# Kernel optimization log

Hardware: AMD Instinct MI355X
Metric: run time of the kernel (lower is better)

Reference implementation:

```python
import jax, jax.numpy as jnp
import numpy as np

P, S, C, F, B = 2, 2, 64, 64, 64


def setup_inputs() -> dict:
    key = jax.random.key(0)
    kx, kq, kw = jax.random.split(key, 3)
    X = jax.random.normal(kx, (B, P * S * C * F), dtype=jnp.float32)
    # sparse connection-strength tensor, densified; nonnegative small values
    dbfc = jax.random.uniform(kq, (P, S, C, F, C, F), dtype=jnp.float32) * 0.01
    wV = jax.random.normal(kw, (F, F), dtype=jnp.float32) * (1.0 / np.sqrt(F))
    return {"X": X, "databaseFeatureConnections": dbfc, "wV": wV}


def reference(X, databaseFeatureConnections, wV):
    p, s, c, f = (databaseFeatureConnections.shape[0], databaseFeatureConnections.shape[1],
                  databaseFeatureConnections.shape[2], databaseFeatureConnections.shape[3])
    b = X.shape[0]
    # wV: nn.Linear(f, f, bias=False) -> x @ W.T
    v = (X.reshape(b, p * s * c, f) @ wV.T).reshape(b, p, s, c, f)
    # kqHead.sum(dim=1).sum(dim=2): collapse both feature axes -> [p, s, c, c]
    scores = databaseFeatureConnections.sum(axis=(3, 5))
    weights = jax.nn.softmax(scores, axis=-1)  # [p, s, c, c]
    # per-head bmm: weights[p,s] @ v[:,p,s] -> [b, c, f] per head; heads concatenated
    # along feature dim in (p outer, s inner) order == reshape of [b, c, p, s, f]
    out = jnp.einsum('pscd,bpsdf->bcpsf', weights, v).reshape(b, c, p * s * f)
    # permute(1, 0, 2) -> [c, b, p*s*f]
    return out.transpose(1, 0, 2)
```

## Files before the change

### kernel.cpp

```cpp
#include <hip/hip_runtime.h>
#include <math.h>


__global__ __launch_bounds__(1024) void scores_softmax_kernel(
    const float* __restrict__ dbfc, float* __restrict__ weights)
{
    const int bid = blockIdx.x;
    const int t   = threadIdx.x;
    const float4* slab = reinterpret_cast<const float4*>(dbfc) + (size_t)bid * (262144 / 4);

    float acc = 0.f;
#pragma unroll 8
    for (int f = 0; f < 64; ++f) {
        float4 v = slab[f * 1024 + t];
        acc += (v.x + v.y) + (v.z + v.w);
    }
#pragma unroll
    for (int m = 1; m < 16; m <<= 1)
        acc += __shfl_xor(acc, m, 64);

    __shared__ float sm[64];
    if ((t & 15) == 0) sm[t >> 4] = acc;
    __syncthreads();

    if (t < 64) {
        float v = sm[t];
        float mx = v;
#pragma unroll
        for (int m = 32; m >= 1; m >>= 1) mx = fmaxf(mx, __shfl_xor(mx, m, 64));
        float e = expf(v - mx);
        float s = e;
#pragma unroll
        for (int m = 32; m >= 1; m >>= 1) s += __shfl_xor(s, m, 64);
        weights[bid * 64 + t] = e / s;
    }
}

__global__ __launch_bounds__(256) void attn_out_kernel(
    const float* __restrict__ X, const float* __restrict__ wV,
    const float* __restrict__ weights, float* __restrict__ out)
{
    const int blk = blockIdx.x;
    const int ps  = blk >> 6;
    const int b   = blk & 63;
    const int t   = threadIdx.x;
    const int tc  = t >> 4;
    const int tf  = t & 15;

    __shared__ float Xs [64][68];
    __shared__ float wVs[64][68];
    __shared__ float Ws [64][68];
    __shared__ float VsT[64][68];

    const float4* xsrc = reinterpret_cast<const float4*>(X + (size_t)b * 16384 + ps * 4096);
    const float4* wsrc = reinterpret_cast<const float4*>(wV);
    const float4* ssrc = reinterpret_cast<const float4*>(weights + ps * 4096);
#pragma unroll
    for (int idx = t; idx < 1024; idx += 256) {
        int r = idx >> 4, j = (idx & 15) * 4;
        *reinterpret_cast<float4*>(&Xs [r][j]) = xsrc[idx];
        *reinterpret_cast<float4*>(&wVs[r][j]) = wsrc[idx];
        *reinterpret_cast<float4*>(&Ws [r][j]) = ssrc[idx];
    }
    __syncthreads();

    float acc[4][4] = {};
    for (int f0 = 0; f0 < 64; f0 += 4) {
        float4 xa[4], wv[4];
#pragma unroll
        for (int ci = 0; ci < 4; ++ci)
            xa[ci] = *reinterpret_cast<const float4*>(&Xs[4 * tc + ci][f0]);
#pragma unroll
        for (int fi = 0; fi < 4; ++fi)
            wv[fi] = *reinterpret_cast<const float4*>(&wVs[tf + 16 * fi][f0]);
#pragma unroll
        for (int ci = 0; ci < 4; ++ci)
#pragma unroll
            for (int fi = 0; fi < 4; ++fi)
                acc[ci][fi] += xa[ci].x * wv[fi].x + xa[ci].y * wv[fi].y
                             + xa[ci].z * wv[fi].z + xa[ci].w * wv[fi].w;
    }
#pragma unroll
    for (int ci = 0; ci < 4; ++ci)
#pragma unroll
        for (int fi = 0; fi < 4; ++fi)
            VsT[tf + 16 * fi][4 * tc + ci] = acc[ci][fi];
    __syncthreads();

    float o[4][4] = {};
    for (int d = 0; d < 64; d += 4) {
        float4 wa[4], va[4];
#pragma unroll
        for (int ci = 0; ci < 4; ++ci)
            wa[ci] = *reinterpret_cast<const float4*>(&Ws[4 * tc + ci][d]);
#pragma unroll
        for (int fi = 0; fi < 4; ++fi)
            va[fi] = *reinterpret_cast<const float4*>(&VsT[tf + 16 * fi][d]);
#pragma unroll
        for (int ci = 0; ci < 4; ++ci)
#pragma unroll
            for (int fi = 0; fi < 4; ++fi)
                o[ci][fi] += wa[ci].x * va[fi].x + wa[ci].y * va[fi].y
                           + wa[ci].z * va[fi].z + wa[ci].w * va[fi].w;
    }

#pragma unroll
    for (int ci = 0; ci < 4; ++ci) {
        const int c = 4 * tc + ci;
        float* orow = out + ((size_t)c * 64 + b) * 256 + ps * 64;
#pragma unroll
        for (int fi = 0; fi < 4; ++fi)
            orow[tf + 16 * fi] = o[ci][fi];
    }
}

extern "C" void kernel_launch(void* const* d_in, const int* in_sizes, int n_in,
                              void* d_out, int out_size, void* d_ws, size_t ws_size,
                              hipStream_t stream)
{
    const float* X    = (const float*)d_in[0];
    const float* dbfc = (const float*)d_in[1];
    const float* wV   = (const float*)d_in[2];
    float* out        = (float*)d_out;
    float* weights    = (float*)d_ws;

    scores_softmax_kernel<<<256, 1024, 0, stream>>>(dbfc, weights);
    attn_out_kernel<<<256, 256, 0, stream>>>(X, wV, weights, out);
}
```

Measured before the change: 64.97 us.

## Split score reduction across more blocks with atomics and move softmax into attention kernel

The dbfc reduction is split from 256 blocks of 1024 threads into 2048 blocks of 256 threads. Each block reduces one chunk with four independent float4 accumulators and atomically adds its partial sums into a zeroed score buffer. The softmax moves into the attention kernel and runs on the shared-memory score tile. This aims to spread the 64 MB streaming read over more CUs and raise memory-level parallelism. The cost is an extra memset launch, float atomics with nondeterministic summation order, and softmax work repeated in every attention block.

Measured after the change: 59.91 us. 7.8% less time.

```diff
diff --git a/kernel.cpp b/kernel.cpp
--- a/kernel.cpp
+++ b/kernel.cpp
@@ -2,43 +2,52 @@
 #include <math.h>
 
 
-__global__ __launch_bounds__(1024) void scores_softmax_kernel(
-    const float* __restrict__ dbfc, float* __restrict__ weights)
+__global__ __launch_bounds__(256) void scores_partial_kernel(
+    const float* __restrict__ dbfc, float* __restrict__ scores)
 {
-    const int bid = blockIdx.x;
-    const int t   = threadIdx.x;
-    const float4* slab = reinterpret_cast<const float4*>(dbfc) + (size_t)bid * (262144 / 4);
+    const int bid   = blockIdx.x;
+    const int slab  = bid >> 3;
+    const int chunk = bid & 7;
+    const int t     = threadIdx.x;
 
-    float acc = 0.f;
-#pragma unroll 8
-    for (int f = 0; f < 64; ++f) {
-        float4 v = slab[f * 1024 + t];
-        acc += (v.x + v.y) + (v.z + v.w);
+    const float4* src = reinterpret_cast<const float4*>(dbfc)
+                      + (size_t)slab * 65536 + chunk * 8192 + t;
+
+    float4 a0 = make_float4(0.f, 0.f, 0.f, 0.f), a1 = a0, a2 = a0, a3 = a0;
+#pragma unroll 2
+    for (int i = 0; i < 32; i += 4) {
+        float4 v0 = src[(i + 0) * 256];
+        float4 v1 = src[(i + 1) * 256];
+        float4 v2 = src[(i + 2) * 256];
+        float4 v3 = src[(i + 3) * 256];
+        a0.x += v0.x; a0.y += v0.y; a0.z += v0.z; a0.w += v0.w;
+        a1.x += v1.x; a1.y += v1.y; a1.z += v1.z; a1.w += v1.w;
+        a2.x += v2.x; a2.y += v2.y; a2.z += v2.z; a2.w += v2.w;
+        a3.x += v3.x; a3.y += v3.y; a3.z += v3.z; a3.w += v3.w;
     }
+    float s0 = (a0.x + a0.y) + (a0.z + a0.w);
+    float s1 = (a1.x + a1.y) + (a1.z + a1.w);
+    float s2 = (a2.x + a2.y) + (a2.z + a2.w);
+    float s3 = (a3.x + a3.y) + (a3.z + a3.w);
 #pragma unroll
-    for (int m = 1; m < 16; m <<= 1)
-        acc += __shfl_xor(acc, m, 64);
-
-    __shared__ float sm[64];
-    if ((t & 15) == 0) sm[t >> 4] = acc;
-    __syncthreads();
-
-    if (t < 64) {
-        float v = sm[t];
-        float mx = v;
-#pragma unroll
-        for (int m = 32; m >= 1; m >>= 1) mx = fmaxf(mx, __shfl_xor(mx, m, 64));
-        float e = expf(v - mx);
-        float s = e;
-#pragma unroll
-        for (int m = 32; m >= 1; m >>= 1) s += __shfl_xor(s, m, 64);
-        weights[bid * 64 + t] = e / s;
+    for (int m = 1; m < 16; m <<= 1) {
+        s0 += __shfl_xor(s0, m, 64);
+        s1 += __shfl_xor(s1, m, 64);
+        s2 += __shfl_xor(s2, m, 64);
+        s3 += __shfl_xor(s3, m, 64);
+    }
+    if ((t & 15) == 0) {
+        float* dst = scores + slab * 64 + (t >> 4);
+        atomicAdd(dst +  0, s0);
+        atomicAdd(dst + 16, s1);
+        atomicAdd(dst + 32, s2);
+        atomicAdd(dst + 48, s3);
     }
 }
 
 __global__ __launch_bounds__(256) void attn_out_kernel(
     const float* __restrict__ X, const float* __restrict__ wV,
-    const float* __restrict__ weights, float* __restrict__ out)
+    const float* __restrict__ scores, float* __restrict__ out)
 {
     const int blk = blockIdx.x;
     const int ps  = blk >> 6;
@@ -54,7 +63,7 @@
 
     const float4* xsrc = reinterpret_cast<const float4*>(X + (size_t)b * 16384 + ps * 4096);
     const float4* wsrc = reinterpret_cast<const float4*>(wV);
-    const float4* ssrc = reinterpret_cast<const float4*>(weights + ps * 4096);
+    const float4* ssrc = reinterpret_cast<const float4*>(scores + ps * 4096);
 #pragma unroll
     for (int idx = t; idx < 1024; idx += 256) {
         int r = idx >> 4, j = (idx & 15) * 4;
@@ -80,6 +89,25 @@
                 acc[ci][fi] += xa[ci].x * wv[fi].x + xa[ci].y * wv[fi].y
                              + xa[ci].z * wv[fi].z + xa[ci].w * wv[fi].w;
     }
+
+    {
+        const int row = t >> 2, q = (t & 3) * 16;
+        float e[16];
+        float mx = -INFINITY;
+#pragma unroll
+        for (int i = 0; i < 16; ++i) mx = fmaxf(mx, Ws[row][q + i]);
+        mx = fmaxf(mx, __shfl_xor(mx, 1, 64));
+        mx = fmaxf(mx, __shfl_xor(mx, 2, 64));
+        float sum = 0.f;
+#pragma unroll
+        for (int i = 0; i < 16; ++i) { e[i] = expf(Ws[row][q + i] - mx); sum += e[i]; }
+        sum += __shfl_xor(sum, 1, 64);
+        sum += __shfl_xor(sum, 2, 64);
+        const float rinv = 1.0f / sum;
+#pragma unroll
+        for (int i = 0; i < 16; ++i) Ws[row][q + i] = e[i] * rinv;
+    }
+
 #pragma unroll
     for (int ci = 0; ci < 4; ++ci)
 #pragma unroll
@@ -122,8 +150,9 @@
     const float* dbfc = (const float*)d_in[1];
     const float* wV   = (const float*)d_in[2];
     float* out        = (float*)d_out;
-    float* weights    = (float*)d_ws;
+    float* scores     = (float*)d_ws;
 
-    scores_softmax_kernel<<<256, 1024, 0, stream>>>(dbfc, weights);
-    attn_out_kernel<<<256, 256, 0, stream>>>(X, wV, weights, out);
+    hipMemsetAsync(scores, 0, 4 * 64 * 64 * sizeof(float), stream);
+    scores_partial_kernel<<<2048, 256, 0, stream>>>(dbfc, scores);
+    attn_out_kernel<<<256, 256, 0, stream>>>(X, wV, scores, out);
 }
```
